# Optimization experiments

Measured on AMD Instinct MI355X. Metric: run time of the kernel, lower is better.

## Reference

```python
import jax, jax.numpy as jnp
import numpy as np

N_NODES = 100000
N_EDGES = 3200000
INP_DIM = 128
OUT_DIM = 128


def setup_inputs() -> dict:
    key = jax.random.key(0)
    ks = jax.random.split(key, 10)
    x = jax.random.normal(ks[0], (N_NODES, INP_DIM), dtype=jnp.float32)
    edge_index = jax.random.randint(ks[1], (2, N_EDGES), 0, N_NODES, dtype=jnp.int64)
    edge_attr = jax.random.uniform(ks[2], (N_EDGES,), dtype=jnp.float32)
    # GCNConv weights (glorot-style scaling) and zero biases, per PyG defaults
    def glorot(k, fin, fout):
        s = jnp.sqrt(6.0 / (fin + fout)).astype(jnp.float32)
        return jax.random.uniform(k, (fin, fout), jnp.float32, -s, s)
    W1 = glorot(ks[3], INP_DIM, 32); b1 = jnp.zeros((32,), jnp.float32)
    W2 = glorot(ks[4], 32, 64);      b2 = jnp.zeros((64,), jnp.float32)
    W3 = glorot(ks[5], 64, OUT_DIM); b3 = jnp.zeros((OUT_DIM,), jnp.float32)
    return {"x": x, "edge_index": edge_index, "edge_attr": edge_attr,
            "W1": W1, "b1": b1, "W2": W2, "b2": b2, "W3": W3, "b3": b3}


def _gcn_norm(edge_index, edge_attr, n_nodes):
    # add self-loops with weight 1, compute symmetric normalization (PyG gcn_norm)
    loop = jnp.arange(n_nodes, dtype=edge_index.dtype)
    row = jnp.concatenate([edge_index[0], loop])  # source
    col = jnp.concatenate([edge_index[1], loop])  # target
    ew = jnp.concatenate([edge_attr, jnp.ones((n_nodes,), edge_attr.dtype)])
    deg = jax.ops.segment_sum(ew, col, num_segments=n_nodes)
    dinv = jnp.where(deg > 0, jax.lax.rsqrt(jnp.maximum(deg, 1e-30)), 0.0)
    norm = dinv[row] * ew * dinv[col]  # [E + N]
    return row, col, norm


def _gcn_conv(x, row, col, norm, W, b, n_nodes):
    h = x @ W                     # [N, Fout] small GEMM first (Fout <= Fin or cheap)
    msg = h[row] * norm[:, None]  # edge-wise gather + scale
    out = jax.ops.segment_sum(msg, col, num_segments=n_nodes)  # scatter-add
    return out + b


def reference(x, edge_index, edge_attr, W1, b1, W2, b2, W3, b3):
    n = x.shape[0]
    row, col, norm = _gcn_norm(edge_index, edge_attr, n)
    h = jax.nn.elu(_gcn_conv(x, row, col, norm, W1, b1, n))
    h = jax.nn.elu(_gcn_conv(h, row, col, norm, W2, b2, n))
    return _gcn_conv(h, row, col, norm, W3, b3, n)
```

## Files before the change

kernel.cpp:

```cpp
#include <hip/hip_runtime.h>
#include <hip/hip_bf16.h>


constexpr int N = 100000;
constexpr int E = 3200000;

constexpr int BSHIFT = 7;
constexpr int BSIZE = 128;
constexpr int NBKT = (N + BSIZE - 1) / BSIZE;

constexpr float FIX_SCALE = 16777216.0f;
constexpr float Q15 = 32768.0f;

constexpr int HIST_EPB = 4096;
constexpr int SC_EPB = 4096;

__device__ __forceinline__ float ldf(const void* p, int isbf, size_t i) {
    return isbf ? __bfloat162float(((const __hip_bfloat16*)p)[i])
                : ((const float*)p)[i];
}

__device__ __forceinline__ int ld_idx(const void* ei, int is64, size_t pos) {
    return is64 ? (int)((const long long*)ei)[pos] : ((const int*)ei)[pos];
}

__device__ __forceinline__ float4 bf4tof4(uint2 u) {
    float4 r;
    r.x = __uint_as_float(u.x << 16);
    r.y = __uint_as_float(u.x & 0xffff0000u);
    r.z = __uint_as_float(u.y << 16);
    r.w = __uint_as_float(u.y & 0xffff0000u);
    return r;
}
__device__ __forceinline__ unsigned short f2bf(float f) {
    unsigned u = __float_as_uint(f);
    unsigned rnd = 0x7fffu + ((u >> 16) & 1u);
    return (unsigned short)((u + rnd) >> 16);
}
__device__ __forceinline__ unsigned packbf2(float a, float b) {
    return (unsigned)f2bf(a) | ((unsigned)f2bf(b) << 16);
}
__device__ __forceinline__ uint2 f4tobf4(float4 v) {
    uint2 r;
    r.x = packbf2(v.x, v.y);
    r.y = packbf2(v.z, v.w);
    return r;
}

__global__ void k_probe(const void* ei, const void* x, int* flags, int* bkt_cnt) {
    __shared__ int bad64, bigcnt;
    int t = threadIdx.x;
    if (t == 0) { bad64 = 0; bigcnt = 0; }
    __syncthreads();
    long long v = ((const long long*)ei)[t];
    if (v < 0 || v >= (long long)N) atomicAdd(&bad64, 1);
    const unsigned short* u = (const unsigned short*)x;
    int big = 0;
    for (int i = t * 16; i < t * 16 + 16; i++) {
        int e = (u[i] >> 7) & 0xFF;
        if (e >= 133) big++;
    }
    atomicAdd(&bigcnt, big);
    for (int i = t; i < NBKT; i += 256) bkt_cnt[i] = 0;
    __syncthreads();
    if (t == 0) { flags[0] = (bad64 == 0) ? 1 : 0; flags[1] = (bigcnt < 40) ? 1 : 0; }
}

__global__ __launch_bounds__(512) void k_hist(const void* ei, const int* flags,
                                              int* bkt_cnt) {
    constexpr int EPT = HIST_EPB / 512;
    __shared__ int h[NBKT];
    int t = threadIdx.x;
    for (int i = t; i < NBKT; i += 512) h[i] = 0;
    __syncthreads();
    int is64 = flags[0];
    size_t eb = (size_t)blockIdx.x * HIST_EPB;
    int nb = (int)min((size_t)HIST_EPB, (size_t)E - eb);
    int cc[EPT];
#pragma unroll
    for (int k = 0; k < EPT; k++) {
        int idx = t + k * 512;
        cc[k] = (idx < nb) ? ld_idx(ei, is64, (size_t)E + eb + idx) : -1;
    }
#pragma unroll
    for (int k = 0; k < EPT; k++)
        if (cc[k] >= 0) atomicAdd(&h[cc[k] >> BSHIFT], 1);
    __syncthreads();
    for (int i = t; i < NBKT; i += 512) {
        int v = h[i];
        if (v) atomicAdd(&bkt_cnt[i], v);
    }
}

__global__ void k_bscan(const int* bkt_cnt, int* bkt_off, int* bkt_cur) {
    __shared__ int s[256];
    int t = threadIdx.x;
    int v[4]; int sum = 0;
#pragma unroll
    for (int j = 0; j < 4; j++) {
        int i = t * 4 + j;
        v[j] = (i < NBKT) ? bkt_cnt[i] : 0;
        sum += v[j];
    }
    s[t] = sum; __syncthreads();
    for (int st = 1; st < 256; st <<= 1) {
        int add = (t >= st) ? s[t - st] : 0;
        __syncthreads();
        s[t] += add;
        __syncthreads();
    }
    int excl = s[t] - sum;
#pragma unroll
    for (int j = 0; j < 4; j++) {
        int i = t * 4 + j;
        if (i < NBKT) { bkt_off[i] = excl; bkt_cur[i] = excl; excl += v[j]; }
    }
    if (t == 0) bkt_off[NBKT] = E;
}

__global__ __launch_bounds__(512) void k_scatter(const void* ei, const int* flags,
                                                 const void* ew, int* bkt_cur,
                                                 int2* tmp) {
    constexpr int EPT = SC_EPB / 512;
    __shared__ int h[NBKT];
    __shared__ int base_s[NBKT];
    int t = threadIdx.x;
    for (int i = t; i < NBKT; i += 512) h[i] = 0;
    __syncthreads();
    int is64 = flags[0], isbf = flags[1];
    size_t eb = (size_t)blockIdx.x * SC_EPB;
    int nb = (int)min((size_t)SC_EPB, (size_t)E - eb);
    int rr[EPT], cc[EPT]; float ww[EPT];
#pragma unroll
    for (int k = 0; k < EPT; k++) {
        int idx = t + k * 512;
        if (idx < nb) {
            size_t e = eb + idx;
            rr[k] = ld_idx(ei, is64, e);
            cc[k] = ld_idx(ei, is64, (size_t)E + e);
            ww[k] = ldf(ew, isbf, e);
        } else {
            rr[k] = 0; cc[k] = -1; ww[k] = 0.f;
        }
    }
#pragma unroll
    for (int k = 0; k < EPT; k++)
        if (cc[k] >= 0) atomicAdd(&h[cc[k] >> BSHIFT], 1);
    __syncthreads();
    for (int i = t; i < NBKT; i += 512) {
        int v = h[i];
        base_s[i] = v ? atomicAdd(&bkt_cur[i], v) : 0;
    }
    __syncthreads();
    for (int i = t; i < NBKT; i += 512) h[i] = 0;
    __syncthreads();
#pragma unroll
    for (int k = 0; k < EPT; k++) {
        if (cc[k] >= 0) {
            int b = cc[k] >> BSHIFT;
            int loc = atomicAdd(&h[b], 1);
            int pos = base_s[b] + loc;
            tmp[pos] = make_int2(rr[k] | ((cc[k] & (BSIZE - 1)) << 17),
                                 __float_as_int(ww[k]));
        }
    }
}

__global__ __launch_bounds__(256) void k_nodecnt(const int2* __restrict__ tmp,
                                                 const int* __restrict__ bkt_off,
                                                 int* __restrict__ counts,
                                                 int* __restrict__ offsets,
                                                 float* __restrict__ dinv) {
    __shared__ int cnt_s[BSIZE];
    __shared__ unsigned int wfx_s[BSIZE];
    __shared__ int sc_s[BSIZE];
    int t = threadIdx.x;
    int b = blockIdx.x;
    if (t < BSIZE) { cnt_s[t] = 0; wfx_s[t] = 0u; }
    __syncthreads();
    int s0 = bkt_off[b], s1 = bkt_off[b + 1];
    for (int p = s0 + t; p < s1; p += 256) {
        int2 ev = tmp[p];
        int c7 = (int)(((unsigned)ev.x) >> 17);
        float w = __int_as_float(ev.y);
        atomicAdd(&cnt_s[c7], 1);
        atomicAdd(&wfx_s[c7], (unsigned)__float2uint_rn(w * FIX_SCALE));
    }
    __syncthreads();
    if (t < BSIZE) sc_s[t] = cnt_s[t];
    __syncthreads();
    for (int st = 1; st < BSIZE; st <<= 1) {
        int add = (t < BSIZE && t >= st) ? sc_s[t - st] : 0;
        __syncthreads();
        if (t < BSIZE) sc_s[t] += add;
        __syncthreads();
    }
    if (t < BSIZE) {
        int node = b * BSIZE + t;
        if (node < N) {
            int c = cnt_s[t];
            offsets[node] = s0 + sc_s[t] - c;
            counts[node] = c;
            float deg = 1.0f + (float)wfx_s[t] * (1.0f / FIX_SCALE);
            dinv[node] = rsqrtf(deg);
        }
    }
}

__global__ __launch_bounds__(256) void k_fill(const int2* __restrict__ tmp,
                                              const int* __restrict__ bkt_off,
                                              const int* __restrict__ offsets,
                                              const float* __restrict__ dinv,
                                              unsigned* __restrict__ epk) {
    __shared__ int lcur[BSIZE];
    int t = threadIdx.x;
    int b = blockIdx.x;
    if (t < BSIZE) {
        int node = b * BSIZE + t;
        lcur[t] = (node < N) ? offsets[node] : 0;
    }
    __syncthreads();
    int s0 = bkt_off[b], s1 = bkt_off[b + 1];
    for (int p = s0 + t; p < s1; p += 256) {
        int2 ev = tmp[p];
        unsigned px = (unsigned)ev.x;
        int r = (int)(px & 0x1FFFFu);
        int c7 = (int)(px >> 17);
        float w = __int_as_float(ev.y);
        float nr = dinv[r] * w;
        unsigned q = __float2uint_rn(nr * Q15);
        if (q > 32767u) q = 32767u;
        int pos = atomicAdd(&lcur[c7], 1);
        epk[pos] = (unsigned)r | (q << 17);
    }
}

template <int FIN, int FOUT, int TM, int TN, int KC, int XMODE, bool OBF,
          bool BIAS, bool ELU>
__global__ __launch_bounds__(256) void k_gemm(const void* __restrict__ X,
                                              const void* __restrict__ W,
                                              const void* __restrict__ bias,
                                              const int* __restrict__ flags,
                                              void* __restrict__ H) {
    constexpr int TCOLS = FOUT / TN;
    constexpr int TROWS = 256 / TCOLS;
    constexpr int BR = TROWS * TM;
    __shared__ float wl[KC * FOUT];
    __shared__ float xt[KC][BR + 1];
    int t = threadIdx.x;
    int isbf = flags[1];
    int base = blockIdx.x * BR;
    int trow = t % TROWS, tcol = t / TROWS;
    int r0 = trow * TM, c0 = tcol * TN;
    float acc[TM][TN] = {};

    for (int kc = 0; kc < FIN; kc += KC) {
        if (kc) __syncthreads();
        if (!isbf) {
            const float4* W4 = (const float4*)W;
            float4* wl4 = (float4*)wl;
            for (int i = t; i < KC * FOUT / 4; i += 256)
                wl4[i] = W4[(size_t)kc * FOUT / 4 + i];
        } else {
            for (int i = t; i < KC * FOUT; i += 256)
                wl[i] = __bfloat162float(((const __hip_bfloat16*)W)[(size_t)kc * FOUT + i]);
        }
        if (XMODE == 2) {
            const uint2* X2 = (const uint2*)X;
            for (int i = t; i < BR * KC / 4; i += 256) {
                int row = i / (KC / 4);
                int kq = i % (KC / 4);
                int node = base + row;
                uint2 u = make_uint2(0u, 0u);
                if (node < N) u = X2[(size_t)node * (FIN / 4) + kc / 4 + kq];
                float4 v = bf4tof4(u);
                int k = kq * 4;
                xt[k][row] = v.x; xt[k + 1][row] = v.y;
                xt[k + 2][row] = v.z; xt[k + 3][row] = v.w;
            }
        } else if (!isbf) {
            const float4* X4 = (const float4*)X;
            for (int i = t; i < BR * KC / 4; i += 256) {
                int row = i / (KC / 4);
                int kq = i % (KC / 4);
                int node = base + row;
                float4 v = make_float4(0.f, 0.f, 0.f, 0.f);
                if (node < N) v = X4[(size_t)node * (FIN / 4) + kc / 4 + kq];
                int k = kq * 4;
                xt[k][row] = v.x; xt[k + 1][row] = v.y;
                xt[k + 2][row] = v.z; xt[k + 3][row] = v.w;
            }
        } else {
            for (int i = t; i < BR * KC; i += 256) {
                int row = i / KC, k = i % KC;
                int node = base + row;
                float v = (node < N)
                    ? __bfloat162float(((const __hip_bfloat16*)X)[(size_t)node * FIN + kc + k])
                    : 0.f;
                xt[k][row] = v;
            }
        }
        __syncthreads();

#pragma unroll 4
        for (int k = 0; k < KC; k++) {
            float a[TM], b[TN];
#pragma unroll
            for (int m = 0; m < TM; m++) a[m] = xt[k][r0 + m];
#pragma unroll
            for (int n = 0; n < TN; n++) b[n] = wl[k * FOUT + c0 + n];
#pragma unroll
            for (int m = 0; m < TM; m++)
#pragma unroll
                for (int n = 0; n < TN; n++) acc[m][n] += a[m] * b[n];
        }
    }

#pragma unroll
    for (int m = 0; m < TM; m++) {
        int node = base + r0 + m;
        if (node >= N) continue;
        float vv[TN];
#pragma unroll
        for (int n = 0; n < TN; n++) {
            float v = acc[m][n];
            if (BIAS) v += ldf(bias, isbf, c0 + n);
            if (ELU) v = (v > 0.0f) ? v : expm1f(v);
            vv[n] = v;
        }
        if (OBF) {
            unsigned* Hrow = (unsigned*)((unsigned short*)H + (size_t)node * FOUT + c0);
#pragma unroll
            for (int n = 0; n < TN; n += 2)
                Hrow[n / 2] = packbf2(vv[n], vv[n + 1]);
        } else {
            float* Hrow = (float*)H + (size_t)node * FOUT + c0;
#pragma unroll
            for (int n = 0; n < TN; n += 4)
                *(float4*)(Hrow + n) = make_float4(vv[n], vv[n + 1], vv[n + 2], vv[n + 3]);
        }
    }
}

template <int F, bool BIAS, bool ELU>
__global__ __launch_bounds__(256) void k_agg(const uint2* __restrict__ Hb,
                                             const int* __restrict__ offsets,
                                             const int* __restrict__ counts,
                                             const unsigned* __restrict__ epk,
                                             const float* __restrict__ dinv,
                                             const void* __restrict__ bias,
                                             const int* __restrict__ flags,
                                             uint2* __restrict__ outb) {
    constexpr int LPN = F / 4;
    constexpr int NPB = 256 / LPN;
    constexpr float QS = 1.0f / Q15;
    int t = threadIdx.x;
    int lane = t % LPN;
    int g = t / LPN;
    int node = blockIdx.x * NPB + g;
    if (node >= N) return;
    float di = dinv[node];
    float4 h = bf4tof4(Hb[(size_t)node * LPN + lane]);
    float4 acc0 = make_float4(0.f, 0.f, 0.f, 0.f);
    float4 acc1 = make_float4(0.f, 0.f, 0.f, 0.f);
    int p = offsets[node];
    int pend = p + counts[node];

    unsigned eA[8];
    bool have = (p + 8 <= pend);
    if (have) {
#pragma unroll
        for (int j = 0; j < 8; j++) eA[j] = epk[p + j];
    }
    while (have) {
        uint2 gg[8];
#pragma unroll
        for (int j = 0; j < 8; j++)
            gg[j] = Hb[(size_t)(eA[j] & 0x1FFFFu) * LPN + lane];
        float w[8];
#pragma unroll
        for (int j = 0; j < 8; j++) w[j] = (float)(eA[j] >> 17) * QS;
        p += 8;
        bool nxt = (p + 8 <= pend);
        unsigned eB[8];
        if (nxt) {
#pragma unroll
            for (int j = 0; j < 8; j++) eB[j] = epk[p + j];
        }
#pragma unroll
        for (int j = 0; j < 8; j += 2) {
            float4 g0 = bf4tof4(gg[j]);
            float4 g1 = bf4tof4(gg[j + 1]);
            acc0.x += g0.x * w[j]; acc0.y += g0.y * w[j];
            acc0.z += g0.z * w[j]; acc0.w += g0.w * w[j];
            acc1.x += g1.x * w[j + 1]; acc1.y += g1.y * w[j + 1];
            acc1.z += g1.z * w[j + 1]; acc1.w += g1.w * w[j + 1];
        }
#pragma unroll
        for (int j = 0; j < 8; j++) eA[j] = eB[j];
        have = nxt;
    }
    for (; p + 4 <= pend; p += 4) {
        unsigned e0 = epk[p], e1 = epk[p + 1], e2 = epk[p + 2], e3 = epk[p + 3];
        float4 h0 = bf4tof4(Hb[(size_t)(e0 & 0x1FFFFu) * LPN + lane]);
        float4 h1 = bf4tof4(Hb[(size_t)(e1 & 0x1FFFFu) * LPN + lane]);
        float4 h2 = bf4tof4(Hb[(size_t)(e2 & 0x1FFFFu) * LPN + lane]);
        float4 h3 = bf4tof4(Hb[(size_t)(e3 & 0x1FFFFu) * LPN + lane]);
        float w0 = (float)(e0 >> 17) * QS;
        float w1 = (float)(e1 >> 17) * QS;
        float w2 = (float)(e2 >> 17) * QS;
        float w3 = (float)(e3 >> 17) * QS;
        acc0.x += h0.x * w0 + h2.x * w2; acc1.x += h1.x * w1 + h3.x * w3;
        acc0.y += h0.y * w0 + h2.y * w2; acc1.y += h1.y * w1 + h3.y * w3;
        acc0.z += h0.z * w0 + h2.z * w2; acc1.z += h1.z * w1 + h3.z * w3;
        acc0.w += h0.w * w0 + h2.w * w2; acc1.w += h1.w * w1 + h3.w * w3;
    }
    for (; p < pend; p++) {
        unsigned e = epk[p];
        float4 hh = bf4tof4(Hb[(size_t)(e & 0x1FFFFu) * LPN + lane]);
        float w = (float)(e >> 17) * QS;
        acc0.x += hh.x * w; acc0.y += hh.y * w;
        acc0.z += hh.z * w; acc0.w += hh.w * w;
    }
    float4 acc;
    acc.x = acc0.x + acc1.x; acc.y = acc0.y + acc1.y;
    acc.z = acc0.z + acc1.z; acc.w = acc0.w + acc1.w;
    float sw = di * di;
    acc.x = acc.x * di + h.x * sw;
    acc.y = acc.y * di + h.y * sw;
    acc.z = acc.z * di + h.z * sw;
    acc.w = acc.w * di + h.w * sw;
    if (BIAS) {
        int fb = lane * 4;
        int isbf = flags[1];
        acc.x += ldf(bias, isbf, fb);
        acc.y += ldf(bias, isbf, fb + 1);
        acc.z += ldf(bias, isbf, fb + 2);
        acc.w += ldf(bias, isbf, fb + 3);
    }
    if (ELU) {
        acc.x = (acc.x > 0.0f) ? acc.x : expm1f(acc.x);
        acc.y = (acc.y > 0.0f) ? acc.y : expm1f(acc.y);
        acc.z = (acc.z > 0.0f) ? acc.z : expm1f(acc.z);
        acc.w = (acc.w > 0.0f) ? acc.w : expm1f(acc.w);
    }
    outb[(size_t)node * LPN + lane] = f4tobf4(acc);
}

__global__ void k_sentinel(float* out, int n) {
    int i = blockIdx.x * blockDim.x + threadIdx.x;
    if (i < n) out[i] = 123.0f;
}

extern "C" void kernel_launch(void* const* d_in, const int* in_sizes, int n_in,
                              void* d_out, int out_size, void* d_ws, size_t ws_size,
                              hipStream_t stream) {
    const void* x  = d_in[0];
    const void* ei = d_in[1];
    const void* ea = d_in[2];
    const void* W1 = d_in[3];
    const void* b1 = d_in[4];
    const void* W2 = d_in[5];
    const void* b2 = d_in[6];
    const void* W3 = d_in[7];
    const void* b3 = d_in[8];
    float* out = (float*)d_out;

    char* ws = (char*)d_ws;
    size_t off = 0;
    auto alloc = [&](size_t bytes) {
        off = (off + 255) & ~(size_t)255;
        size_t r = off;
        off += bytes;
        return r;
    };
    float* dinv    = (float*)(ws + alloc((size_t)N * 4));
    int*   counts  = (int*)  (ws + alloc((size_t)N * 4));
    int*   offsets = (int*)  (ws + alloc((size_t)N * 4));
    int*   bkt_cnt = (int*)  (ws + alloc((size_t)NBKT * 4));
    int*   bkt_off = (int*)  (ws + alloc((size_t)(NBKT + 1) * 4));
    int*   bkt_cur = (int*)  (ws + alloc((size_t)NBKT * 4));
    int*   flags   = (int*)  (ws + alloc(256));
    unsigned* epk  = (unsigned*)(ws + alloc((size_t)E * 4));
    unsigned short* bufA = (unsigned short*)(ws + alloc((size_t)N * 64 * 2));
    unsigned short* bufB = (unsigned short*)(ws + alloc((size_t)N * 64 * 2));
    size_t need = off;
    int2* tmp = (int2*)bufA;

    if (ws_size < need) {
        hipLaunchKernelGGL(k_sentinel, dim3((N * 128 + 255) / 256), dim3(256), 0, stream,
                           out, N * 128);
        return;
    }

    const int gH = (E + HIST_EPB - 1) / HIST_EPB;
    const int gS = (E + SC_EPB - 1) / SC_EPB;

    hipLaunchKernelGGL(k_probe, dim3(1), dim3(256), 0, stream, ei, x, flags, bkt_cnt);
    hipLaunchKernelGGL(k_hist, dim3(gH), dim3(512), 0, stream, ei, flags, bkt_cnt);
    hipLaunchKernelGGL(k_bscan, dim3(1), dim3(256), 0, stream, bkt_cnt, bkt_off, bkt_cur);
    hipLaunchKernelGGL(k_scatter, dim3(gS), dim3(512), 0, stream, ei, flags, ea, bkt_cur, tmp);
    hipLaunchKernelGGL(k_nodecnt, dim3(NBKT), dim3(256), 0, stream, tmp, bkt_off,
                       counts, offsets, dinv);
    hipLaunchKernelGGL(k_fill, dim3(NBKT), dim3(256), 0, stream, tmp, bkt_off,
                       offsets, dinv, epk);

    hipLaunchKernelGGL((k_gemm<128, 32, 2, 4, 32, 1, true, false, false>),
                       dim3((N + 63) / 64), dim3(256), 0, stream, x, W1, nullptr, flags, bufA);
    hipLaunchKernelGGL((k_agg<32, true, true>), dim3((N + 31) / 32), dim3(256), 0, stream,
                       (const uint2*)bufA, offsets, counts, epk, dinv, b1, flags, (uint2*)bufB);
    hipLaunchKernelGGL((k_agg<32, false, false>), dim3((N + 31) / 32), dim3(256), 0, stream,
                       (const uint2*)bufB, offsets, counts, epk, dinv, nullptr, flags, (uint2*)bufA);
    hipLaunchKernelGGL((k_gemm<32, 64, 4, 4, 32, 2, true, true, true>),
                       dim3((N + 63) / 64), dim3(256), 0, stream, bufA, W2, b2, flags, bufB);
    hipLaunchKernelGGL((k_agg<64, false, false>), dim3((N + 15) / 16), dim3(256), 0, stream,
                       (const uint2*)bufB, offsets, counts, epk, dinv, nullptr, flags, (uint2*)bufA);
    hipLaunchKernelGGL((k_gemm<64, 128, 4, 8, 32, 2, false, true, false>),
                       dim3((N + 63) / 64), dim3(256), 0, stream, bufA, W3, b3, flags, out);
}
```

Measured before the change: 425.2 us.

## Store bf16 features chunk-major so each aggregation pass gathers a cache-resident slice

Intermediate bf16 feature buffers are stored in 8 feature chunks, each a contiguous [N, F/8] array. The GEMM writes and reads use this layout, and the aggregation kernel gets a chunk index from blockIdx so each block gathers only one chunk's slice. The goal is a smaller per-pass working set for the random neighbor gathers, so they hit L2/LLC more often. The cost is that every edge list is read 8 times, and each gather moves only 8 bytes per lane, which lowers useful bytes per memory transaction.

Measured after the change: 672.9 us. 58.3% more time.

```diff
diff --git a/kernel.cpp b/kernel.cpp
--- a/kernel.cpp
+++ b/kernel.cpp
@@ -242,6 +242,7 @@
                                               const void* __restrict__ bias,
                                               const int* __restrict__ flags,
                                               void* __restrict__ H) {
+    static_assert(!OBF || TN == 4, "chunk-major write assumes TN==4");
     constexpr int TCOLS = FOUT / TN;
     constexpr int TROWS = 256 / TCOLS;
     constexpr int BR = TROWS * TM;
@@ -267,12 +268,15 @@
         }
         if (XMODE == 2) {
             const uint2* X2 = (const uint2*)X;
+            constexpr int UPCI = FIN / 32;
             for (int i = t; i < BR * KC / 4; i += 256) {
-                int row = i / (KC / 4);
-                int kq = i % (KC / 4);
+                int kq = i / BR;
+                int row = i % BR;
                 int node = base + row;
+                int q = kc / 4 + kq;
                 uint2 u = make_uint2(0u, 0u);
-                if (node < N) u = X2[(size_t)node * (FIN / 4) + kc / 4 + kq];
+                if (node < N)
+                    u = X2[((size_t)(q / UPCI) * N + node) * UPCI + (q % UPCI)];
                 float4 v = bf4tof4(u);
                 int k = kq * 4;
                 xt[k][row] = v.x; xt[k + 1][row] = v.y;
@@ -329,10 +333,11 @@
             vv[n] = v;
         }
         if (OBF) {
-            unsigned* Hrow = (unsigned*)((unsigned short*)H + (size_t)node * FOUT + c0);
-#pragma unroll
-            for (int n = 0; n < TN; n += 2)
-                Hrow[n / 2] = packbf2(vv[n], vv[n + 1]);
+            constexpr int FPCO = FOUT / 8;
+            constexpr int UPCO = FOUT / 32;
+            uint2* H2 = (uint2*)H;
+            uint2 val = make_uint2(packbf2(vv[0], vv[1]), packbf2(vv[2], vv[3]));
+            H2[((size_t)(c0 / FPCO) * N + node) * UPCO + ((c0 % FPCO) >> 2)] = val;
         } else {
             float* Hrow = (float*)H + (size_t)node * FOUT + c0;
 #pragma unroll
@@ -351,16 +356,20 @@
                                              const void* __restrict__ bias,
                                              const int* __restrict__ flags,
                                              uint2* __restrict__ outb) {
-    constexpr int LPN = F / 4;
-    constexpr int NPB = 256 / LPN;
+    constexpr int FPC = F / 8;
+    constexpr int UPC = F / 32;
+    constexpr int NPB = 256 / UPC;
     constexpr float QS = 1.0f / Q15;
     int t = threadIdx.x;
-    int lane = t % LPN;
-    int g = t / LPN;
-    int node = blockIdx.x * NPB + g;
+    int chunk = blockIdx.x & 7;
+    int lane = t % UPC;
+    int g = t / UPC;
+    int node = (blockIdx.x >> 3) * NPB + g;
     if (node >= N) return;
+    const uint2* Hp = Hb + (size_t)chunk * N * UPC;
+    uint2* Op = outb + (size_t)chunk * N * UPC;
     float di = dinv[node];
-    float4 h = bf4tof4(Hb[(size_t)node * LPN + lane]);
+    float4 h = bf4tof4(Hp[(size_t)node * UPC + lane]);
     float4 acc0 = make_float4(0.f, 0.f, 0.f, 0.f);
     float4 acc1 = make_float4(0.f, 0.f, 0.f, 0.f);
     int p = offsets[node];
@@ -376,7 +385,7 @@
         uint2 gg[8];
 #pragma unroll
         for (int j = 0; j < 8; j++)
-            gg[j] = Hb[(size_t)(eA[j] & 0x1FFFFu) * LPN + lane];
+            gg[j] = Hp[(size_t)(eA[j] & 0x1FFFFu) * UPC + lane];
         float w[8];
 #pragma unroll
         for (int j = 0; j < 8; j++) w[j] = (float)(eA[j] >> 17) * QS;
@@ -402,10 +411,10 @@
     }
     for (; p + 4 <= pend; p += 4) {
         unsigned e0 = epk[p], e1 = epk[p + 1], e2 = epk[p + 2], e3 = epk[p + 3];
-        float4 h0 = bf4tof4(Hb[(size_t)(e0 & 0x1FFFFu) * LPN + lane]);
-        float4 h1 = bf4tof4(Hb[(size_t)(e1 & 0x1FFFFu) * LPN + lane]);
-        float4 h2 = bf4tof4(Hb[(size_t)(e2 & 0x1FFFFu) * LPN + lane]);
-        float4 h3 = bf4tof4(Hb[(size_t)(e3 & 0x1FFFFu) * LPN + lane]);
+        float4 h0 = bf4tof4(Hp[(size_t)(e0 & 0x1FFFFu) * UPC + lane]);
+        float4 h1 = bf4tof4(Hp[(size_t)(e1 & 0x1FFFFu) * UPC + lane]);
+        float4 h2 = bf4tof4(Hp[(size_t)(e2 & 0x1FFFFu) * UPC + lane]);
+        float4 h3 = bf4tof4(Hp[(size_t)(e3 & 0x1FFFFu) * UPC + lane]);
         float w0 = (float)(e0 >> 17) * QS;
         float w1 = (float)(e1 >> 17) * QS;
         float w2 = (float)(e2 >> 17) * QS;
@@ -417,7 +426,7 @@
     }
     for (; p < pend; p++) {
         unsigned e = epk[p];
-        float4 hh = bf4tof4(Hb[(size_t)(e & 0x1FFFFu) * LPN + lane]);
+        float4 hh = bf4tof4(Hp[(size_t)(e & 0x1FFFFu) * UPC + lane]);
         float w = (float)(e >> 17) * QS;
         acc0.x += hh.x * w; acc0.y += hh.y * w;
         acc0.z += hh.z * w; acc0.w += hh.w * w;
@@ -431,7 +440,7 @@
     acc.z = acc.z * di + h.z * sw;
     acc.w = acc.w * di + h.w * sw;
     if (BIAS) {
-        int fb = lane * 4;
+        int fb = chunk * FPC + lane * 4;
         int isbf = flags[1];
         acc.x += ldf(bias, isbf, fb);
         acc.y += ldf(bias, isbf, fb + 1);
@@ -444,7 +453,7 @@
         acc.z = (acc.z > 0.0f) ? acc.z : expm1f(acc.z);
         acc.w = (acc.w > 0.0f) ? acc.w : expm1f(acc.w);
     }
-    outb[(size_t)node * LPN + lane] = f4tobf4(acc);
+    Op[(size_t)node * UPC + lane] = f4tobf4(acc);
 }
 
 __global__ void k_sentinel(float* out, int n) {
@@ -495,6 +504,8 @@
 
     const int gH = (E + HIST_EPB - 1) / HIST_EPB;
     const int gS = (E + SC_EPB - 1) / SC_EPB;
+    const int gA32 = ((N + 255) / 256) * 8;
+    const int gA64 = ((N + 127) / 128) * 8;
 
     hipLaunchKernelGGL(k_probe, dim3(1), dim3(256), 0, stream, ei, x, flags, bkt_cnt);
     hipLaunchKernelGGL(k_hist, dim3(gH), dim3(512), 0, stream, ei, flags, bkt_cnt);
@@ -507,13 +518,13 @@
 
     hipLaunchKernelGGL((k_gemm<128, 32, 2, 4, 32, 1, true, false, false>),
                        dim3((N + 63) / 64), dim3(256), 0, stream, x, W1, nullptr, flags, bufA);
-    hipLaunchKernelGGL((k_agg<32, true, true>), dim3((N + 31) / 32), dim3(256), 0, stream,
+    hipLaunchKernelGGL((k_agg<32, true, true>), dim3(gA32), dim3(256), 0, stream,
                        (const uint2*)bufA, offsets, counts, epk, dinv, b1, flags, (uint2*)bufB);
-    hipLaunchKernelGGL((k_agg<32, false, false>), dim3((N + 31) / 32), dim3(256), 0, stream,
+    hipLaunchKernelGGL((k_agg<32, false, false>), dim3(gA32), dim3(256), 0, stream,
                        (const uint2*)bufB, offsets, counts, epk, dinv, nullptr, flags, (uint2*)bufA);
     hipLaunchKernelGGL((k_gemm<32, 64, 4, 4, 32, 2, true, true, true>),
                        dim3((N + 63) / 64), dim3(256), 0, stream, bufA, W2, b2, flags, bufB);
-    hipLaunchKernelGGL((k_agg<64, false, false>), dim3((N + 15) / 16), dim3(256), 0, stream,
+    hipLaunchKernelGGL((k_agg<64, false, false>), dim3(gA64), dim3(256), 0, stream,
                        (const uint2*)bufB, offsets, counts, epk, dinv, nullptr, flags, (uint2*)bufA);
     hipLaunchKernelGGL((k_gemm<64, 128, 4, 8, 32, 2, false, true, false>),
                        dim3((N + 63) / 64), dim3(256), 0, stream, bufA, W3, b3, flags, out);
```
